# Performance work log

Measured on AMD Instinct MI355X. Metric: run time of the kernel, lower is better.

The kernel has to match this reference:

```python
import jax, jax.numpy as jnp
import numpy as np

DISCOUNT = 0.997
LAMBDA = 0.95
LOSS_SCALE = 0.5
NUM_BINS = 255
BIN_LO, BIN_HI = -20.0, 20.0


def setup_inputs() -> dict:
    key = jax.random.key(0)
    k0, k1, k2, k3 = jax.random.split(key, 4)
    B, H, D = 1024, 16, 4096
    latents = jax.random.normal(k0, (B, H, D), dtype=jnp.float32)
    rewards = jax.random.normal(k1, (B, H), dtype=jnp.float32)
    dones = jnp.zeros((B, H), dtype=jnp.float32)
    bootstrap_latent = jax.random.normal(k2, (B, D), dtype=jnp.float32)
    W = jax.random.normal(k3, (D, NUM_BINS), dtype=jnp.float32) * (1.0 / np.sqrt(D))
    b = jnp.zeros((NUM_BINS,), dtype=jnp.float32)
    return {"latents": latents, "rewards": rewards, "dones": dones,
            "bootstrap_latent": bootstrap_latent, "W": W, "b": b}


def _bin_centers():
    return jnp.linspace(BIN_LO, BIN_HI, NUM_BINS, dtype=jnp.float32)


def _value_head(x, W, b):
    # x: (N, D) -> logits (N, K), value (N,)
    logits = x @ W + b
    value = jax.nn.softmax(logits, axis=-1) @ _bin_centers()
    return value, logits


def _target_to_bins(returns_flat):
    # two-hot encoding onto uniform bins; returns (N, K) soft target
    step = (BIN_HI - BIN_LO) / (NUM_BINS - 1)
    pos = (jnp.clip(returns_flat, BIN_LO, BIN_HI) - BIN_LO) / step  # in [0, K-1]
    low = jnp.clip(jnp.floor(pos).astype(jnp.int32), 0, NUM_BINS - 2)
    frac = pos - low.astype(pos.dtype)
    oh_lo = jax.nn.one_hot(low, NUM_BINS, dtype=returns_flat.dtype)
    oh_hi = jax.nn.one_hot(low + 1, NUM_BINS, dtype=returns_flat.dtype)
    return (1.0 - frac)[:, None] * oh_lo + frac[:, None] * oh_hi


def _lambda_returns(rewards, values, dones, bootstrap_value):
    # backward linear recurrence: G_t = r_t + gamma*mask_t*((1-lam)*V_{t+1} + lam*G_{t+1})
    next_values = jnp.concatenate([values[:, 1:], bootstrap_value[:, None]], axis=1)
    xs = (rewards.T, next_values.T, (1.0 - dones).T)  # time-major (H, B)

    def step(carry, x):
        r, nv, m = x
        g = r + DISCOUNT * m * ((1.0 - LAMBDA) * nv + LAMBDA * carry)
        return g, g

    _, outs = jax.lax.scan(step, bootstrap_value, xs, reverse=True)
    return outs.T  # (B, H)


def reference(latents, rewards, dones, bootstrap_latent, W, b):
    B, H = rewards.shape
    flat_latents = latents.reshape(-1, latents.shape[-1])  # (B*H, D)
    values_flat, logits = _value_head(flat_latents, W, b)
    values = values_flat.reshape(B, H)

    bootstrap_value, _ = _value_head(bootstrap_latent, W, b)
    bootstrap_value = jax.lax.stop_gradient(bootstrap_value)

    returns = jax.lax.stop_gradient(
        _lambda_returns(rewards, jax.lax.stop_gradient(values), dones, bootstrap_value))

    target = _target_to_bins(returns.reshape(-1))  # (B*H, K)
    logp = jax.nn.log_softmax(logits, axis=-1)
    value_loss = jnp.mean(-jnp.sum(target * logp, axis=-1))
    total_loss = LOSS_SCALE * value_loss

    return jnp.stack([total_loss, value_loss, values.mean(), returns.mean(),
                      jnp.std(values, ddof=1), jnp.std(returns, ddof=1)])
```

## Files before the change

### kernel.cpp

```cpp
#include <hip/hip_runtime.h>
#include <math.h>

#define NBINS 255
#define BIN_LO_F (-20.0f)
#define BIN_HI_F (20.0f)

typedef __attribute__((ext_vector_type(8))) short short8;
typedef __attribute__((ext_vector_type(16))) float f32x16;

__device__ __forceinline__ unsigned short f2bf(float f) {
    unsigned u = __builtin_bit_cast(unsigned, f);
    unsigned r = u + 0x7fffu + ((u >> 16) & 1u);
    return (unsigned short)(r >> 16);
}

__device__ __forceinline__ unsigned pkbf(float lo, float hi) {
    unsigned d;
    asm("v_cvt_pk_bf16_f32 %0, %1, %2" : "=v"(d) : "v"(lo), "v"(hi));
    return d;
}

__device__ __forceinline__ short8 mk8(unsigned a, unsigned b, unsigned c, unsigned d) {
    union { unsigned u[4]; short8 s; } t;
    t.u[0] = a; t.u[1] = b; t.u[2] = c; t.u[3] = d;
    return t.s;
}

__device__ __forceinline__ void glds16(const void* g, void* l) {
    __builtin_amdgcn_global_load_lds(
        (const __attribute__((address_space(1))) unsigned int*)g,
        (__attribute__((address_space(3))) unsigned int*)l, 16, 0, 0);
}

__device__ __forceinline__ double wave_reduce_sum_d(double v) {
    #pragma unroll
    for (int m = 32; m >= 1; m >>= 1) v += __shfl_xor(v, m, 64);
    return v;
}

__global__ __launch_bounds__(256) void pack_w7(
    const float* __restrict__ W, char* __restrict__ Wimg)
{
    int u = blockIdx.x * 256 + threadIdx.x;
    int kt = u >> 10;
    int v  = u & 1023;
    int ks = v >> 9;
    int lh = (v >> 8) & 1;
    int col = v & 255;
    int k0  = kt * 32 + ks * 16 + lh * 8;
    short8 s;
    #pragma unroll
    for (int e = 0; e < 8; ++e)
        s[e] = (col < NBINS) ? (short)f2bf(W[(size_t)(k0 + e) * NBINS + col]) : (short)0;
    *(short8*)(Wimg + (size_t)u * 16) = s;
}

__global__ __launch_bounds__(512, 2) void gemm_mfma_v17(
    const float* __restrict__ latents, const float* __restrict__ boot,
    const char* __restrict__ Wimg, float* __restrict__ P, size_t Pstride,
    int NR, int R, int D, int split, int nMt, int nwg8)
{
    __shared__ __align__(16) char ldsA[2][16384];
    __shared__ __align__(16) char ldsB[2][16384];

    const int tid  = threadIdx.x;
    const int wave = tid >> 6, lane = tid & 63;
    const int l31  = lane & 31, lhi = lane >> 5;
    const int mw   = wave & 1, nw = wave >> 1;
    const int KQ   = D / split;
    const int NT   = KQ >> 5;

    int bid  = blockIdx.x;
    int work = (bid & 7) * nwg8 + (bid >> 3);
    const int kq = work / nMt;
    const int mt = work - kq * nMt;
    const int row0 = mt * 128;
    float* __restrict__ Pq = P + (size_t)kq * Pstride;

    const float* Abase = (row0 < NR) ? latents + (size_t)row0 * D
                                     : boot + (size_t)(row0 - NR) * D;

    const int au  = lane & 7;
    const int rl0 = (wave << 4) + 0 + (lane >> 3);
    const int rl1 = (wave << 4) + 8 + (lane >> 3);
    const float* asrc0 = Abase + (size_t)rl0 * D + kq * KQ + ((au ^ (rl0 & 7)) << 2);
    const float* asrc1 = Abase + (size_t)rl1 * D + kq * KQ + ((au ^ (rl1 & 7)) << 2);
    const int adst0 = (wave << 11) + 0    + (lane << 4);
    const int adst1 = (wave << 11) + 1024 + (lane << 4);

    const char* bsrc = Wimg + ((size_t)kq * NT) * 16384 + (wave << 11) + (lane << 4);
    const int bdst0 = (wave << 11) + (lane << 4);

    f32x16 acc[2][2];
    #pragma unroll
    for (int rg = 0; rg < 2; ++rg)
        #pragma unroll
        for (int cg = 0; cg < 2; ++cg)
            #pragma unroll
            for (int r = 0; r < 16; ++r) acc[rg][cg][r] = 0.f;

    const int ar0 = mw * 64 + l31;
    const int ar1 = ar0 + 32;
    const int ax  = ar0 & 7;
    const int boff = (lhi << 12) + ((nw * 64 + l31) << 4);

#define STAGE(T, BUF) do {                                                  \
        const size_t ko_ = (size_t)(T) * 32;                                \
        glds16(asrc0 + ko_, &ldsA[BUF][adst0]);                             \
        glds16(asrc1 + ko_, &ldsA[BUF][adst1]);                             \
        const char* bs_ = bsrc + (size_t)(T) * 16384;                       \
        glds16(bs_,        &ldsB[BUF][bdst0]);                              \
        glds16(bs_ + 1024, &ldsB[BUF][bdst0 + 1024]);                       \
    } while (0)

#define COMPUTE(BUF) do {                                                   \
        _Pragma("unroll")                                                   \
        for (int ks = 0; ks < 2; ++ks) {                                    \
            const int u0_ = ks * 4 + lhi * 2;                               \
            float4 f0_ = *(const float4*)(&ldsA[BUF][ar0 * 128 + ((u0_       ^ ax) << 4)]); \
            float4 f1_ = *(const float4*)(&ldsA[BUF][ar0 * 128 + (((u0_ + 1) ^ ax) << 4)]); \
            float4 g0_ = *(const float4*)(&ldsA[BUF][ar1 * 128 + ((u0_       ^ ax) << 4)]); \
            float4 g1_ = *(const float4*)(&ldsA[BUF][ar1 * 128 + (((u0_ + 1) ^ ax) << 4)]); \
            short8 a0_ = mk8(pkbf(f0_.x, f0_.y), pkbf(f0_.z, f0_.w),        \
                             pkbf(f1_.x, f1_.y), pkbf(f1_.z, f1_.w));       \
            short8 a1_ = mk8(pkbf(g0_.x, g0_.y), pkbf(g0_.z, g0_.w),        \
                             pkbf(g1_.x, g1_.y), pkbf(g1_.z, g1_.w));       \
            short8 b0_ = *(const short8*)(&ldsB[BUF][(ks << 13) + boff]);   \
            short8 b1_ = *(const short8*)(&ldsB[BUF][(ks << 13) + boff + 512]); \
            acc[0][0] = __builtin_amdgcn_mfma_f32_32x32x16_bf16(a0_, b0_, acc[0][0], 0, 0, 0); \
            acc[0][1] = __builtin_amdgcn_mfma_f32_32x32x16_bf16(a0_, b1_, acc[0][1], 0, 0, 0); \
            acc[1][0] = __builtin_amdgcn_mfma_f32_32x32x16_bf16(a1_, b0_, acc[1][0], 0, 0, 0); \
            acc[1][1] = __builtin_amdgcn_mfma_f32_32x32x16_bf16(a1_, b1_, acc[1][1], 0, 0, 0); \
        }                                                                   \
    } while (0)

#define BAR()   __builtin_amdgcn_s_barrier()
#define SCHED() __builtin_amdgcn_sched_barrier(0)
#define WAITV4() asm volatile("s_waitcnt vmcnt(4)" ::: "memory")
#define WAITV0() asm volatile("s_waitcnt vmcnt(0)" ::: "memory")

    STAGE(0, 0);

    int t = 0;
    for (; t + 3 < NT; t += 2) {
        BAR(); SCHED(); STAGE(t + 1, 1); SCHED(); WAITV4(); BAR(); SCHED(); COMPUTE(0);
        BAR(); SCHED(); STAGE(t + 2, 0); SCHED(); WAITV4(); BAR(); SCHED(); COMPUTE(1);
    }
    BAR(); SCHED(); STAGE(NT - 1, 1); SCHED(); WAITV4(); BAR(); SCHED(); COMPUTE(0);
    BAR(); SCHED(); WAITV0(); BAR(); SCHED(); COMPUTE(1);

#undef STAGE
#undef COMPUTE
#undef BAR
#undef SCHED
#undef WAITV4
#undef WAITV0

    #pragma unroll
    for (int rg = 0; rg < 2; ++rg) {
        #pragma unroll
        for (int cg = 0; cg < 2; ++cg) {
            int col = nw * 64 + cg * 32 + l31;
            if (col < NBINS) {
                #pragma unroll
                for (int r = 0; r < 16; ++r) {
                    int row = row0 + mw * 64 + rg * 32 + (r & 3) + 8 * (r >> 2) + 4 * lhi;
                    Pq[(size_t)row * 256 + col] = acc[rg][cg][r];
                }
            }
        }
    }
}

__global__ __launch_bounds__(256) void softmax_statsN(
    const float* __restrict__ P, size_t Pstride, int split,
    const float* __restrict__ bvec, float* __restrict__ values,
    float* __restrict__ logZ, int R)
{
    int row  = blockIdx.x * 4 + (threadIdx.x >> 6);
    int lane = threadIdx.x & 63;
    if (row >= R) return;
    const float* pr = P + (size_t)row * 256;
    const float step = (float)(40.0 / 254.0);

    float l[4];
    float m = -INFINITY;
    #pragma unroll
    for (int u = 0; u < 4; ++u) {
        int idx = lane + 64 * u;
        if (idx < NBINS) {
            float s = bvec[idx];
            for (int q = 0; q < split; ++q) s += pr[(size_t)q * Pstride + idx];
            l[u] = s;
        } else l[u] = -INFINITY;
        m = fmaxf(m, l[u]);
    }
    #pragma unroll
    for (int sh = 32; sh >= 1; sh >>= 1) m = fmaxf(m, __shfl_xor(m, sh, 64));

    float s = 0.f, sc = 0.f;
    #pragma unroll
    for (int u = 0; u < 4; ++u) {
        int idx = lane + 64 * u;
        if (idx < NBINS) {
            float e = __expf(l[u] - m);
            s  += e;
            sc += e * (BIN_LO_F + step * (float)idx);
        }
    }
    #pragma unroll
    for (int sh = 32; sh >= 1; sh >>= 1) {
        s  += __shfl_xor(s, sh, 64);
        sc += __shfl_xor(sc, sh, 64);
    }
    if (lane == 0) {
        values[row] = sc / s;
        logZ[row]   = m + __logf(s);
    }
}

__global__ void lambda_returns_k(
    const float* __restrict__ rewards, const float* __restrict__ dones,
    const float* __restrict__ values, float* __restrict__ returns,
    int B, int H, int NR)
{
    int b = blockIdx.x * blockDim.x + threadIdx.x;
    if (b >= B) return;
    const float gamma = 0.997f;
    const float lam   = 0.95f;
    const float oml   = (float)(1.0 - 0.95);
    float bootv = values[NR + b];
    float g = bootv;
    for (int h = H - 1; h >= 0; --h) {
        float nv   = (h == H - 1) ? bootv : values[b * H + h + 1];
        float mask = 1.0f - dones[b * H + h];
        g = rewards[b * H + h] + gamma * mask * (oml * nv + lam * g);
        returns[b * H + h] = g;
    }
}

__global__ __launch_bounds__(256) void loss_momentsN(
    const float* __restrict__ P, size_t Pstride, int split,
    const float* __restrict__ bvec, const float* __restrict__ logZ,
    const float* __restrict__ values, const float* __restrict__ returns,
    double* __restrict__ accum, int NR)
{
    int row = blockIdx.x * blockDim.x + threadIdx.x;
    double lsum = 0, vsum = 0, v2 = 0, rsum = 0, r2 = 0;
    if (row < NR) {
        float v   = values[row];
        float ret = returns[row];
        float cl  = fminf(fmaxf(ret, BIN_LO_F), BIN_HI_F);
        const float step = (float)(40.0 / 254.0);
        float pos = (cl - BIN_LO_F) / step;
        int low = (int)floorf(pos);
        low = min(max(low, 0), NBINS - 2);
        float frac = pos - (float)low;
        size_t base = (size_t)row * 256;
        float llo = bvec[low], lhi = bvec[low + 1];
        for (int q = 0; q < split; ++q) {
            llo += P[(size_t)q * Pstride + base + low];
            lhi += P[(size_t)q * Pstride + base + low + 1];
        }
        float loss = logZ[row] - (1.f - frac) * llo - frac * lhi;
        lsum = (double)loss;
        vsum = (double)v;   v2 = (double)v * (double)v;
        rsum = (double)ret; r2 = (double)ret * (double)ret;
    }
    lsum = wave_reduce_sum_d(lsum);
    vsum = wave_reduce_sum_d(vsum);
    v2   = wave_reduce_sum_d(v2);
    rsum = wave_reduce_sum_d(rsum);
    r2   = wave_reduce_sum_d(r2);
    if ((threadIdx.x & 63) == 0) {
        atomicAdd(&accum[0], lsum);
        atomicAdd(&accum[1], vsum);
        atomicAdd(&accum[2], v2);
        atomicAdd(&accum[3], rsum);
        atomicAdd(&accum[4], r2);
    }
}

__global__ void finalize_k(const double* __restrict__ accum,
                           float* __restrict__ out, int NR)
{
    if (threadIdx.x == 0 && blockIdx.x == 0) {
        double n  = (double)NR;
        double vl = accum[0] / n;
        double mv = accum[1] / n;
        double vv = (accum[2] - n * mv * mv) / (n - 1.0);
        double mr = accum[3] / n;
        double vr = (accum[4] - n * mr * mr) / (n - 1.0);
        out[0] = (float)(0.5 * vl);
        out[1] = (float)vl;
        out[2] = (float)mv;
        out[3] = (float)mr;
        out[4] = (float)sqrt(vv > 0.0 ? vv : 0.0);
        out[5] = (float)sqrt(vr > 0.0 ? vr : 0.0);
    }
}

extern "C" void kernel_launch(void* const* d_in, const int* in_sizes, int n_in,
                              void* d_out, int out_size, void* d_ws, size_t ws_size,
                              hipStream_t stream) {
    const float* latents = (const float*)d_in[0];
    const float* rewards = (const float*)d_in[1];
    const float* dones   = (const float*)d_in[2];
    const float* boot    = (const float*)d_in[3];
    const float* W       = (const float*)d_in[4];
    const float* bvec    = (const float*)d_in[5];
    float* out = (float*)d_out;

    const int BH = in_sizes[1];
    const int D  = in_sizes[0] / BH;
    const int B  = in_sizes[3] / D;
    const int H  = BH / B;
    const int NR = BH;
    const int R  = NR + B;

    const size_t Pstride = (size_t)R * 256;
    const size_t fixed   = (size_t)R * 2 * 4 + (size_t)NR * 4 + 512 +
                           (size_t)(D / 32) * 16384 + 4096;
    int split = (ws_size >= 4 * Pstride * 4 + fixed) ? 4 : 2;

    char* ws = (char*)d_ws;
    size_t off = 0;
    float* P = (float*)(ws + off); off += (size_t)split * Pstride * sizeof(float);
    float* values = (float*)(ws + off); off += (size_t)R * sizeof(float);
    float* logZ   = (float*)(ws + off); off += (size_t)R * sizeof(float);
    float* rets   = (float*)(ws + off); off += (size_t)NR * sizeof(float);
    off = (off + 255) & ~(size_t)255;
    double* accum = (double*)(ws + off); off += 64;
    off = (off + 255) & ~(size_t)255;
    char* Wimg    = ws + off; off += (size_t)(D / 32) * 16384;

    hipMemsetAsync(accum, 0, 64, stream);

    const int packUnits = (D / 32) * 1024;
    pack_w7<<<packUnits / 256, 256, 0, stream>>>(W, Wimg);

    const int nMt = R / 128;
    const int nwg = nMt * split;
    gemm_mfma_v17<<<nwg, 512, 0, stream>>>(latents, boot, Wimg, P, Pstride,
                                           NR, R, D, split, nMt, nwg / 8);
    softmax_statsN<<<(R + 3) / 4, 256, 0, stream>>>(P, Pstride, split, bvec,
                                                    values, logZ, R);
    lambda_returns_k<<<(B + 255) / 256, 256, 0, stream>>>(rewards, dones, values, rets, B, H, NR);
    loss_momentsN<<<(NR + 255) / 256, 256, 0, stream>>>(P, Pstride, split, bvec, logZ,
                                                        values, rets, accum, NR);
    finalize_k<<<1, 64, 0, stream>>>(accum, out, NR);
}
```

Baseline: 176.7 us.

## Use 256-row GEMM tiles with 16 waves, larger K-split, and bf16 partials

The GEMM workgroup grows to 1024 threads covering 256 rows, so each B tile in LDS is shared by twice as many rows and each wave stages only one B chunk. The K dimension is split 8 or 16 ways instead of 2 or 4 to keep enough workgroups in flight. Partial logits are stored as bf16 to cut the memory traffic from the larger split, and the softmax and loss kernels widen them back. In exchange it loses precision in the summed partial logits, and launch_bounds(1024,4) with 96KB of LDS per block may not reach the requested occupancy.

```diff
diff --git a/kernel.cpp b/kernel.cpp
--- a/kernel.cpp
+++ b/kernel.cpp
@@ -12,6 +12,11 @@
     unsigned u = __builtin_bit_cast(unsigned, f);
     unsigned r = u + 0x7fffu + ((u >> 16) & 1u);
     return (unsigned short)(r >> 16);
+}
+
+__device__ __forceinline__ float bf2f(unsigned short s) {
+    unsigned u = ((unsigned)s) << 16;
+    return __builtin_bit_cast(float, u);
 }
 
 __device__ __forceinline__ unsigned pkbf(float lo, float hi) {
@@ -55,18 +60,18 @@
     *(short8*)(Wimg + (size_t)u * 16) = s;
 }
 
-__global__ __launch_bounds__(512, 2) void gemm_mfma_v17(
+__global__ __launch_bounds__(1024, 4) void gemm_mfma_v18(
     const float* __restrict__ latents, const float* __restrict__ boot,
-    const char* __restrict__ Wimg, float* __restrict__ P, size_t Pstride,
+    const char* __restrict__ Wimg, unsigned short* __restrict__ P, size_t Pstride,
     int NR, int R, int D, int split, int nMt, int nwg8)
 {
-    __shared__ __align__(16) char ldsA[2][16384];
+    __shared__ __align__(16) char ldsA[2][32768];
     __shared__ __align__(16) char ldsB[2][16384];
 
     const int tid  = threadIdx.x;
     const int wave = tid >> 6, lane = tid & 63;
     const int l31  = lane & 31, lhi = lane >> 5;
-    const int mw   = wave & 1, nw = wave >> 1;
+    const int mw   = wave & 3, nw = wave >> 2;
     const int KQ   = D / split;
     const int NT   = KQ >> 5;
 
@@ -74,8 +79,8 @@
     int work = (bid & 7) * nwg8 + (bid >> 3);
     const int kq = work / nMt;
     const int mt = work - kq * nMt;
-    const int row0 = mt * 128;
-    float* __restrict__ Pq = P + (size_t)kq * Pstride;
+    const int row0 = mt * 256;
+    unsigned short* __restrict__ Pq = P + (size_t)kq * Pstride;
 
     const float* Abase = (row0 < NR) ? latents + (size_t)row0 * D
                                      : boot + (size_t)(row0 - NR) * D;
@@ -88,8 +93,8 @@
     const int adst0 = (wave << 11) + 0    + (lane << 4);
     const int adst1 = (wave << 11) + 1024 + (lane << 4);
 
-    const char* bsrc = Wimg + ((size_t)kq * NT) * 16384 + (wave << 11) + (lane << 4);
-    const int bdst0 = (wave << 11) + (lane << 4);
+    const char* bsrc = Wimg + ((size_t)kq * NT) * 16384 + (wave << 10) + (lane << 4);
+    const int bdst0 = (wave << 10) + (lane << 4);
 
     f32x16 acc[2][2];
     #pragma unroll
@@ -108,9 +113,7 @@
         const size_t ko_ = (size_t)(T) * 32;                                \
         glds16(asrc0 + ko_, &ldsA[BUF][adst0]);                             \
         glds16(asrc1 + ko_, &ldsA[BUF][adst1]);                             \
-        const char* bs_ = bsrc + (size_t)(T) * 16384;                       \
-        glds16(bs_,        &ldsB[BUF][bdst0]);                              \
-        glds16(bs_ + 1024, &ldsB[BUF][bdst0 + 1024]);                       \
+        glds16(bsrc + (size_t)(T) * 16384, &ldsB[BUF][bdst0]);              \
     } while (0)
 
 #define COMPUTE(BUF) do {                                                   \
@@ -136,24 +139,24 @@
 
 #define BAR()   __builtin_amdgcn_s_barrier()
 #define SCHED() __builtin_amdgcn_sched_barrier(0)
-#define WAITV4() asm volatile("s_waitcnt vmcnt(4)" ::: "memory")
+#define WAITV3() asm volatile("s_waitcnt vmcnt(3)" ::: "memory")
 #define WAITV0() asm volatile("s_waitcnt vmcnt(0)" ::: "memory")
 
     STAGE(0, 0);
 
     int t = 0;
     for (; t + 3 < NT; t += 2) {
-        BAR(); SCHED(); STAGE(t + 1, 1); SCHED(); WAITV4(); BAR(); SCHED(); COMPUTE(0);
-        BAR(); SCHED(); STAGE(t + 2, 0); SCHED(); WAITV4(); BAR(); SCHED(); COMPUTE(1);
-    }
-    BAR(); SCHED(); STAGE(NT - 1, 1); SCHED(); WAITV4(); BAR(); SCHED(); COMPUTE(0);
+        BAR(); SCHED(); STAGE(t + 1, 1); SCHED(); WAITV3(); BAR(); SCHED(); COMPUTE(0);
+        BAR(); SCHED(); STAGE(t + 2, 0); SCHED(); WAITV3(); BAR(); SCHED(); COMPUTE(1);
+    }
+    BAR(); SCHED(); STAGE(NT - 1, 1); SCHED(); WAITV3(); BAR(); SCHED(); COMPUTE(0);
     BAR(); SCHED(); WAITV0(); BAR(); SCHED(); COMPUTE(1);
 
 #undef STAGE
 #undef COMPUTE
 #undef BAR
 #undef SCHED
-#undef WAITV4
+#undef WAITV3
 #undef WAITV0
 
     #pragma unroll
@@ -165,22 +168,22 @@
                 #pragma unroll
                 for (int r = 0; r < 16; ++r) {
                     int row = row0 + mw * 64 + rg * 32 + (r & 3) + 8 * (r >> 2) + 4 * lhi;
-                    Pq[(size_t)row * 256 + col] = acc[rg][cg][r];
+                    Pq[(size_t)row * 256 + col] = f2bf(acc[rg][cg][r]);
                 }
             }
         }
     }
 }
 
-__global__ __launch_bounds__(256) void softmax_statsN(
-    const float* __restrict__ P, size_t Pstride, int split,
+__global__ __launch_bounds__(256) void softmax_statsB(
+    const unsigned short* __restrict__ P, size_t Pstride, int split,
     const float* __restrict__ bvec, float* __restrict__ values,
     float* __restrict__ logZ, int R)
 {
     int row  = blockIdx.x * 4 + (threadIdx.x >> 6);
     int lane = threadIdx.x & 63;
     if (row >= R) return;
-    const float* pr = P + (size_t)row * 256;
+    const unsigned short* pr = P + (size_t)row * 256;
     const float step = (float)(40.0 / 254.0);
 
     float l[4];
@@ -190,7 +193,7 @@
         int idx = lane + 64 * u;
         if (idx < NBINS) {
             float s = bvec[idx];
-            for (int q = 0; q < split; ++q) s += pr[(size_t)q * Pstride + idx];
+            for (int q = 0; q < split; ++q) s += bf2f(pr[(size_t)q * Pstride + idx]);
             l[u] = s;
         } else l[u] = -INFINITY;
         m = fmaxf(m, l[u]);
@@ -239,8 +242,8 @@
     }
 }
 
-__global__ __launch_bounds__(256) void loss_momentsN(
-    const float* __restrict__ P, size_t Pstride, int split,
+__global__ __launch_bounds__(256) void loss_momentsB(
+    const unsigned short* __restrict__ P, size_t Pstride, int split,
     const float* __restrict__ bvec, const float* __restrict__ logZ,
     const float* __restrict__ values, const float* __restrict__ returns,
     double* __restrict__ accum, int NR)
@@ -259,8 +262,8 @@
         size_t base = (size_t)row * 256;
         float llo = bvec[low], lhi = bvec[low + 1];
         for (int q = 0; q < split; ++q) {
-            llo += P[(size_t)q * Pstride + base + low];
-            lhi += P[(size_t)q * Pstride + base + low + 1];
+            llo += bf2f(P[(size_t)q * Pstride + base + low]);
+            lhi += bf2f(P[(size_t)q * Pstride + base + low + 1]);
         }
         float loss = logZ[row] - (1.f - frac) * llo - frac * lhi;
         lsum = (double)loss;
@@ -321,11 +324,12 @@
     const size_t Pstride = (size_t)R * 256;
     const size_t fixed   = (size_t)R * 2 * 4 + (size_t)NR * 4 + 512 +
                            (size_t)(D / 32) * 16384 + 4096;
-    int split = (ws_size >= 4 * Pstride * 4 + fixed) ? 4 : 2;
+    int split = (ws_size >= 16 * Pstride * 2 + fixed) ? 16 : 8;
 
     char* ws = (char*)d_ws;
     size_t off = 0;
-    float* P = (float*)(ws + off); off += (size_t)split * Pstride * sizeof(float);
+    unsigned short* P = (unsigned short*)(ws + off);
+    off += (size_t)split * Pstride * sizeof(unsigned short);
     float* values = (float*)(ws + off); off += (size_t)R * sizeof(float);
     float* logZ   = (float*)(ws + off); off += (size_t)R * sizeof(float);
     float* rets   = (float*)(ws + off); off += (size_t)NR * sizeof(float);
@@ -339,14 +343,14 @@
     const int packUnits = (D / 32) * 1024;
     pack_w7<<<packUnits / 256, 256, 0, stream>>>(W, Wimg);
 
-    const int nMt = R / 128;
+    const int nMt = R / 256;
     const int nwg = nMt * split;
-    gemm_mfma_v17<<<nwg, 512, 0, stream>>>(latents, boot, Wimg, P, Pstride,
-                                           NR, R, D, split, nMt, nwg / 8);
-    softmax_statsN<<<(R + 3) / 4, 256, 0, stream>>>(P, Pstride, split, bvec,
+    gemm_mfma_v18<<<nwg, 1024, 0, stream>>>(latents, boot, Wimg, P, Pstride,
+                                            NR, R, D, split, nMt, nwg / 8);
+    softmax_statsB<<<(R + 3) / 4, 256, 0, stream>>>(P, Pstride, split, bvec,
                                                     values, logZ, R);
     lambda_returns_k<<<(B + 255) / 256, 256, 0, stream>>>(rewards, dones, values, rets, B, H, NR);
-    loss_momentsN<<<(NR + 255) / 256, 256, 0, stream>>>(P, Pstride, split, bvec, logZ,
+    loss_momentsB<<<(NR + 255) / 256, 256, 0, stream>>>(P, Pstride, split, bvec, logZ,
                                                         values, rets, accum, NR);
     finalize_k<<<1, 64, 0, stream>>>(accum, out, NR);
 }
```

Result: slower. 219.6 us (+24.2%).
